# Kernel tuning notes

Measured on AMD Instinct MI355X. Metric: run time of the kernel, lower is better.

Reference implementation:

```python
import jax, jax.numpy as jnp
import numpy as np
from jax import lax

# Dimensions (see shape_source): CAML on MIMIC-style ICD coding
B, L, D, F, Y, V, K = 8, 2500, 100, 50, 8000, 50002, 9
PAD = K // 2  # floor(kernel_size/2) = 4 -> 'same' length for odd K


def setup_inputs() -> dict:
    key = jax.random.key(0)
    ks = jax.random.split(key, 8)
    x = jax.random.randint(ks[0], (B, L), 0, V)                      # token ids
    target = (jax.random.uniform(ks[1], (B, Y)) < 0.01).astype(jnp.float32)  # sparse multi-label
    embed_W = (jax.random.normal(ks[2], (V, D)) * 0.1).at[0].set(0.0)  # padding_idx=0 row zeroed
    conv_w = jax.random.normal(ks[3], (F, D, K)) * 0.05                # (out_ch, in_ch, k)
    conv_b = jax.random.normal(ks[4], (F,)) * 0.01
    U_w = jax.random.normal(ks[5], (Y, F)) * 0.05                      # attention; nn.Linear weight, bias unused
    final_w = jax.random.normal(ks[6], (Y, F)) * 0.05
    final_b = jax.random.normal(ks[7], (Y,)) * 0.01
    return dict(x=x, target=target, embed_W=embed_W, conv_w=conv_w,
                conv_b=conv_b, U_w=U_w, final_w=final_w, final_b=final_b)


def reference(x, target, embed_W, conv_w, conv_b, U_w, final_w, final_b):
    # embed (dropout is identity at eval)
    e = embed_W[x]                                   # (B, L, D)
    # conv1d over length, 'same' padding, then tanh
    h = lax.conv_general_dilated(
        jnp.transpose(e, (0, 2, 1)), conv_w,
        window_strides=(1,), padding=[(PAD, PAD)],
        dimension_numbers=("NCH", "OIH", "NCH"))
    h = jnp.tanh(h + conv_b[None, :, None])          # (B, F, L)
    h = jnp.transpose(h, (0, 2, 1))                  # (B, L, F)
    # label-wise attention pooling: alpha = softmax(U.weight @ h^T) over L
    scores = jnp.einsum('yf,blf->byl', U_w, h)       # (B, Y, L) -- large intermediate
    alpha = jax.nn.softmax(scores, axis=2)
    m = jnp.einsum('byl,blf->byf', alpha, h)         # (B, Y, F)
    yhat = jnp.sum(final_w[None, :, :] * m, axis=2) + final_b  # (B, Y)
    # F.binary_cross_entropy_with_logits, mean reduction (stable form)
    loss = jnp.mean(jnp.maximum(yhat, 0) - yhat * target + jnp.log1p(jnp.exp(-jnp.abs(yhat))))
    return yhat, loss, alpha
```

## Files before the change

kernel.cpp:

```cpp
#include <hip/hip_runtime.h>
#include <hip/hip_bf16.h>
#include <math.h>

#define BB 8
#define LL 2500
#define LPAD 2560
#define DD 100
#define FF 50
#define FP 64
#define YY 8000
#define KS 9
#define LCH 256
#define NCH 10

typedef __attribute__((ext_vector_type(8))) short short8;
typedef __attribute__((ext_vector_type(4))) float f32x4;
typedef float f32x4u __attribute__((ext_vector_type(4), aligned(4)));

__device__ inline f32x4 mfma_bf16(short8 a, short8 b, f32x4 c) {
    return __builtin_amdgcn_mfma_f32_16x16x32_bf16(a, b, c, 0, 0, 0);
}

__device__ inline unsigned short f2bf(float x) {
    unsigned int u = __builtin_bit_cast(unsigned int, x);
    unsigned int r = u + 0x7fffu + ((u >> 16) & 1u);
    return (unsigned short)(r >> 16);
}

__device__ inline unsigned long long pack4bf(const float* a) {
    return (unsigned long long)f2bf(a[0])
         | ((unsigned long long)f2bf(a[1]) << 16)
         | ((unsigned long long)f2bf(a[2]) << 32)
         | ((unsigned long long)f2bf(a[3]) << 48);
}

__device__ inline float bf2f(unsigned short s) {
    return __builtin_bit_cast(float, (unsigned int)s << 16);
}

__device__ inline float tanhfast(float x) {
    float e = __expf(2.f * x);
    return 1.f - 2.f / (e + 1.f);
}

__global__ void k_prep(const float* __restrict__ cw, unsigned short* __restrict__ wA,
                       const float* __restrict__ Uw, unsigned short* __restrict__ Ub) {
    int i = blockIdx.x * blockDim.x + threadIdx.x;
    if (i < 64 * KS * 128) {
        int f = i / (KS * 128);
        int r = i - f * (KS * 128);
        int kk = r >> 7;
        int d = r & 127;
        float v = (f < FF && d < DD) ? cw[(f * DD + d) * KS + kk] : 0.f;
        wA[i] = f2bf(v);
    }
    if (i < YY * FP) {
        int y = i >> 6, f = i & 63;
        float v = (f < FF) ? Uw[y * FF + f] : 0.f;
        Ub[i] = f2bf(v);
    }
}

__global__ __launch_bounds__(256) void k_conv(const int* __restrict__ x,
                                              const float* __restrict__ embW,
                                              const unsigned short* __restrict__ wA,
                                              const float* __restrict__ cb,
                                              unsigned short* __restrict__ hB,
                                              unsigned short* __restrict__ hT) {
    __shared__ unsigned short eL[72 * 136];
    __shared__ int sX[72];
    int b = blockIdx.x & 7;
    int t = blockIdx.x >> 3;
    int l0 = t * 64;
    int tid = threadIdx.x;

    if (tid < 72) {
        int gl = l0 - 4 + tid;
        sX[tid] = (gl >= 0 && gl < LL) ? x[b * LL + gl] : -1;
    }
    __syncthreads();
    for (int i = tid; i < 72 * 25; i += 256) {
        int row = i / 25, c = i - row * 25;
        int id = sX[row];
        float4 v = make_float4(0.f, 0.f, 0.f, 0.f);
        if (id >= 0) v = *(const float4*)(embW + (size_t)id * DD + c * 4);
        float a[4] = {v.x, v.y, v.z, v.w};
        *(unsigned long long*)&eL[row * 136 + c * 4] = pack4bf(a);
    }
    for (int i = tid; i < 72 * 9; i += 256) {
        int row = i / 9, c = i - row * 9;
        *(unsigned long long*)&eL[row * 136 + 100 + c * 4] = 0ull;
    }
    __syncthreads();

    int w = tid >> 6, lane = tid & 63, lm = lane & 15, g = lane >> 4;
    f32x4 cacc[4];
#pragma unroll
    for (int mt = 0; mt < 4; ++mt) cacc[mt] = (f32x4){0.f, 0.f, 0.f, 0.f};

    for (int kk = 0; kk < KS; ++kk) {
#pragma unroll
        for (int dc = 0; dc < 4; ++dc) {
            short8 bfrag = *(const short8*)&eL[(w * 16 + lm + kk) * 136 + dc * 32 + g * 8];
#pragma unroll
            for (int mt = 0; mt < 4; ++mt) {
                short8 afrag = *(const short8*)(wA + ((mt * 16 + lm) * KS + kk) * 128 + dc * 32 + g * 8);
                cacc[mt] = mfma_bf16(afrag, bfrag, cacc[mt]);
            }
        }
    }

    int l = l0 + w * 16 + lm;
    unsigned long long packs[4];
#pragma unroll
    for (int mt = 0; mt < 4; ++mt) {
        float vals[4];
#pragma unroll
        for (int j = 0; j < 4; ++j) {
            int f = mt * 16 + g * 4 + j;
            vals[j] = (f < FF) ? tanhfast(cacc[mt][j] + cb[f]) : 0.f;
        }
        packs[mt] = pack4bf(vals);
        *(unsigned long long*)&hB[((size_t)b * LPAD + l) * FP + mt * 16 + g * 4] = packs[mt];
    }
    __syncthreads();
    unsigned short* hTile = eL;
#pragma unroll
    for (int mt = 0; mt < 4; ++mt)
#pragma unroll
        for (int j = 0; j < 4; ++j)
            hTile[(mt * 16 + g * 4 + j) * 72 + w * 16 + lm] =
                (unsigned short)(packs[mt] >> (16 * j));
    __syncthreads();
    {
        int f = tid >> 2, q = tid & 3;
        short8 v0 = *(const short8*)&hTile[f * 72 + q * 16];
        short8 v1 = *(const short8*)&hTile[f * 72 + q * 16 + 8];
        unsigned short* dst = hT + ((size_t)b * FP + f) * LPAD + l0 + q * 16;
        *(short8*)dst = v0;
        *(short8*)(dst + 8) = v1;
    }
}

__global__ __launch_bounds__(256, 4) void k_attn7(const unsigned short* __restrict__ hB,
                                                  const unsigned short* __restrict__ hT,
                                                  const unsigned short* __restrict__ Ub,
                                                  const float* __restrict__ fw,
                                                  const float* __restrict__ fb,
                                                  const float* __restrict__ tgt,
                                                  float* __restrict__ out,
                                                  float* __restrict__ lossAcc) {
    __shared__ unsigned short sAB[2][32 * LCH];
    __shared__ float sRed[128];
    __shared__ float sInv[32];

    int b = blockIdx.x & 7;
    int y0 = (blockIdx.x >> 3) * 32;
    int tid = threadIdx.x;
    int w = tid >> 6, lane = tid & 63, lm = lane & 15, g = lane >> 4;

    const unsigned short* hBb = hB + (size_t)b * LPAD * FP;
    const unsigned short* hTb = hT + (size_t)b * FP * LPAD;

    short8 uf[2][2];
#pragma unroll
    for (int yt = 0; yt < 2; ++yt) {
        uf[yt][0] = *(const short8*)(Ub + (size_t)(y0 + yt * 16 + lm) * FP + g * 8);
        uf[yt][1] = *(const short8*)(Ub + (size_t)(y0 + yt * 16 + lm) * FP + 32 + g * 8);
    }

    float ssum[2] = {0.f, 0.f};
    for (int it = 0; it < 40; ++it) {
        int l0 = it * 64 + w * 16;
        const unsigned short* hrow = hBb + (size_t)l0 * FP;
        short8 a0 = *(const short8*)(hrow + lm * FP + g * 8);
        short8 a1 = *(const short8*)(hrow + lm * FP + 32 + g * 8);
#pragma unroll
        for (int yt = 0; yt < 2; ++yt) {
            f32x4 cc = {0.f, 0.f, 0.f, 0.f};
            cc = mfma_bf16(a0, uf[yt][0], cc);
            cc = mfma_bf16(a1, uf[yt][1], cc);
#pragma unroll
            for (int j = 0; j < 4; ++j)
                ssum[yt] += (l0 + g * 4 + j < LL) ? __expf(cc[j]) : 0.f;
        }
    }
#pragma unroll
    for (int yt = 0; yt < 2; ++yt) {
        float s = ssum[yt];
        s += __shfl_xor(s, 16);
        s += __shfl_xor(s, 32);
        if (g == 0) sRed[w * 32 + yt * 16 + lm] = s;
    }
    __syncthreads();
    if (tid < 32)
        sInv[tid] = 1.f / (sRed[tid] + sRed[32 + tid] + sRed[64 + tid] + sRed[96 + tid]);
    __syncthreads();

    f32x4 macc[2][4];
#pragma unroll
    for (int yt = 0; yt < 2; ++yt)
#pragma unroll
        for (int ft = 0; ft < 4; ++ft) macc[yt][ft] = (f32x4){0.f, 0.f, 0.f, 0.f};

    float* alphaBase = out + 64001 + ((size_t)b * YY + y0) * LL;
    int buf = 0;
    for (int c = 0; c < NCH; ++c) {
        char* sw = (char*)sAB[buf];
#pragma unroll
        for (int t = 0; t < 4; ++t) {
            int lt = w * 4 + t;
            int l0 = c * LCH + lt * 16;
            const unsigned short* hrow = hBb + (size_t)l0 * FP;
            short8 a0 = *(const short8*)(hrow + lm * FP + g * 8);
            short8 a1 = *(const short8*)(hrow + lm * FP + 32 + g * 8);
#pragma unroll
            for (int yt = 0; yt < 2; ++yt) {
                f32x4 cc = {0.f, 0.f, 0.f, 0.f};
                cc = mfma_bf16(a0, uf[yt][0], cc);
                cc = mfma_bf16(a1, uf[yt][1], cc);
                float inv = sInv[yt * 16 + lm];
                float av[4];
#pragma unroll
                for (int j = 0; j < 4; ++j)
                    av[j] = (l0 + g * 4 + j < LL) ? __expf(cc[j]) * inv : 0.f;
                int row = yt * 16 + lm;
                int off = row * 512 + ((lt * 32 + g * 8) ^ ((lm & 7) << 4));
                *(unsigned long long*)&sw[off] = pack4bf(av);
            }
        }
        __syncthreads();
#pragma unroll
        for (int rr = 0; rr < 8; ++rr) {
            int row = w * 8 + rr;
            int lc = lane * 4;
            if (c * LCH + lc < LL) {
                unsigned long long pv =
                    *(const unsigned long long*)&sw[row * 512 + ((lane * 8) ^ ((row & 7) << 4))];
                f32x4 v = {bf2f((unsigned short)pv),
                           bf2f((unsigned short)(pv >> 16)),
                           bf2f((unsigned short)(pv >> 32)),
                           bf2f((unsigned short)(pv >> 48))};
                __builtin_nontemporal_store(v,
                    (f32x4u*)(alphaBase + (size_t)row * LL + c * LCH + lc));
            }
        }
#pragma unroll
        for (int i = 0; i < 2; ++i) {
            int kc = w * 2 + i;
            short8 bf[4];
#pragma unroll
            for (int ft = 0; ft < 4; ++ft)
                bf[ft] = *(const short8*)(hTb + (size_t)(ft * 16 + lm) * LPAD + c * LCH + kc * 32 + g * 8);
#pragma unroll
            for (int yt = 0; yt < 2; ++yt) {
                int row = yt * 16 + lm;
                short8 pa = *(const short8*)&sw[row * 512 + ((kc * 64 + g * 16) ^ ((lm & 7) << 4))];
#pragma unroll
                for (int ft = 0; ft < 4; ++ft)
                    macc[yt][ft] = mfma_bf16(pa, bf[ft], macc[yt][ft]);
            }
        }
        buf ^= 1;
    }

#pragma unroll
    for (int yt = 0; yt < 2; ++yt) {
#pragma unroll
        for (int j = 0; j < 4; ++j) {
            int y = y0 + yt * 16 + g * 4 + j;
            float z = 0.f;
#pragma unroll
            for (int ft = 0; ft < 4; ++ft) {
                int f = ft * 16 + lm;
                float fwv = (f < FF) ? fw[(size_t)y * FF + f] : 0.f;
                z += macc[yt][ft][j] * fwv;
            }
            z += __shfl_xor(z, 1);
            z += __shfl_xor(z, 2);
            z += __shfl_xor(z, 4);
            z += __shfl_xor(z, 8);
            if (lm == 0) sRed[w * 32 + yt * 16 + g * 4 + j] = z;
        }
    }
    __syncthreads();
    if (w == 0) {
        float bce = 0.f;
        if (lane < 32) {
            int y = y0 + lane;
            float z = sRed[lane] + sRed[32 + lane] + sRed[64 + lane] + sRed[96 + lane] + fb[y];
            out[b * YY + y] = z;
            float tg = tgt[b * YY + y];
            bce = fmaxf(z, 0.f) - z * tg + log1pf(__expf(-fabsf(z)));
        }
        bce += __shfl_xor(bce, 1);
        bce += __shfl_xor(bce, 2);
        bce += __shfl_xor(bce, 4);
        bce += __shfl_xor(bce, 8);
        bce += __shfl_xor(bce, 16);
        bce += __shfl_xor(bce, 32);
        if (lane == 0) atomicAdd(lossAcc, bce);
    }
}

__global__ void k_loss(const float* __restrict__ acc, float* __restrict__ out) {
    out[64000] = acc[0] / (float)(BB * YY);
}

extern "C" void kernel_launch(void* const* d_in, const int* in_sizes, int n_in,
                              void* d_out, int out_size, void* d_ws, size_t ws_size,
                              hipStream_t stream) {
    const int*   x    = (const int*)d_in[0];
    const float* tgt  = (const float*)d_in[1];
    const float* embW = (const float*)d_in[2];
    const float* cw   = (const float*)d_in[3];
    const float* cb   = (const float*)d_in[4];
    const float* Uw   = (const float*)d_in[5];
    const float* fw   = (const float*)d_in[6];
    const float* fb   = (const float*)d_in[7];
    float* out = (float*)d_out;

    float*          lossAcc = (float*)d_ws;
    unsigned short* wA = (unsigned short*)((char*)d_ws + 256);
    unsigned short* Ub = (unsigned short*)((char*)d_ws + 163840);
    unsigned short* hB = (unsigned short*)((char*)d_ws + 1212416);
    unsigned short* hT = (unsigned short*)((char*)d_ws + 3833856);

    hipMemsetAsync(d_ws, 0, 4, stream);
    k_prep<<<(YY * FP + 255) / 256, 256, 0, stream>>>(cw, wA, Uw, Ub);
    k_conv<<<BB * 40, 256, 0, stream>>>(x, embW, wA, cb, hB, hT);
    k_attn7<<<250 * 8, 256, 0, stream>>>(hB, hT, Ub, fw, fb, tgt, out, lossAcc);
    k_loss<<<1, 1, 0, stream>>>(lossAcc, out);
}
```

Baseline: 307.2 us.

## Split softmax denominator into separate kernel and halve attention L-chunk size

Moves the softmax denominator pass out of the attention kernel into a new k_denom kernel that writes per-(b,y) inverse sums to workspace. The attention kernel then reads these inverses directly and uses 128-wide L chunks instead of 256, which halves LDS usage so the launch bound can rise to 6 blocks per CU. The goal is higher occupancy and less in-kernel synchronization, at the cost of an extra launch and a workspace round trip, while the score matmul and exp for the denominator are still computed once in each kernel.

```diff
diff --git a/kernel.cpp b/kernel.cpp
--- a/kernel.cpp
+++ b/kernel.cpp
@@ -10,8 +10,8 @@
 #define FP 64
 #define YY 8000
 #define KS 9
-#define LCH 256
-#define NCH 10
+#define LCH 128
+#define NCH 20
 
 typedef __attribute__((ext_vector_type(8))) short short8;
 typedef __attribute__((ext_vector_type(4))) float f32x4;
@@ -142,9 +142,41 @@
     }
 }
 
-__global__ __launch_bounds__(256, 4) void k_attn7(const unsigned short* __restrict__ hB,
+__global__ __launch_bounds__(256) void k_denom(const unsigned short* __restrict__ hB,
+                                               const unsigned short* __restrict__ Ub,
+                                               float* __restrict__ invD) {
+    int b = blockIdx.x & 7;
+    int y0 = (blockIdx.x >> 3) * 64;
+    int tid = threadIdx.x;
+    int w = tid >> 6, lane = tid & 63, lm = lane & 15, g = lane >> 4;
+    int ybase = y0 + w * 16;
+
+    const unsigned short* hBb = hB + (size_t)b * LPAD * FP;
+    short8 uf0 = *(const short8*)(Ub + (size_t)(ybase + lm) * FP + g * 8);
+    short8 uf1 = *(const short8*)(Ub + (size_t)(ybase + lm) * FP + 32 + g * 8);
+
+    float ssum = 0.f;
+    for (int it = 0; it < 160; ++it) {
+        int l0 = it * 16;
+        const unsigned short* hrow = hBb + (size_t)l0 * FP;
+        short8 a0 = *(const short8*)(hrow + lm * FP + g * 8);
+        short8 a1 = *(const short8*)(hrow + lm * FP + 32 + g * 8);
+        f32x4 cc = {0.f, 0.f, 0.f, 0.f};
+        cc = mfma_bf16(a0, uf0, cc);
+        cc = mfma_bf16(a1, uf1, cc);
+#pragma unroll
+        for (int j = 0; j < 4; ++j)
+            ssum += (l0 + g * 4 + j < LL) ? __expf(cc[j]) : 0.f;
+    }
+    ssum += __shfl_xor(ssum, 16);
+    ssum += __shfl_xor(ssum, 32);
+    if (g == 0) invD[(size_t)b * YY + ybase + lm] = 1.f / ssum;
+}
+
+__global__ __launch_bounds__(256, 6) void k_attn8(const unsigned short* __restrict__ hB,
                                                   const unsigned short* __restrict__ hT,
                                                   const unsigned short* __restrict__ Ub,
+                                                  const float* __restrict__ invD,
                                                   const float* __restrict__ fw,
                                                   const float* __restrict__ fb,
                                                   const float* __restrict__ tgt,
@@ -152,7 +184,6 @@
                                                   float* __restrict__ lossAcc) {
     __shared__ unsigned short sAB[2][32 * LCH];
     __shared__ float sRed[128];
-    __shared__ float sInv[32];
 
     int b = blockIdx.x & 7;
     int y0 = (blockIdx.x >> 3) * 32;
@@ -163,39 +194,13 @@
     const unsigned short* hTb = hT + (size_t)b * FP * LPAD;
 
     short8 uf[2][2];
+    float inv[2];
 #pragma unroll
     for (int yt = 0; yt < 2; ++yt) {
         uf[yt][0] = *(const short8*)(Ub + (size_t)(y0 + yt * 16 + lm) * FP + g * 8);
         uf[yt][1] = *(const short8*)(Ub + (size_t)(y0 + yt * 16 + lm) * FP + 32 + g * 8);
-    }
-
-    float ssum[2] = {0.f, 0.f};
-    for (int it = 0; it < 40; ++it) {
-        int l0 = it * 64 + w * 16;
-        const unsigned short* hrow = hBb + (size_t)l0 * FP;
-        short8 a0 = *(const short8*)(hrow + lm * FP + g * 8);
-        short8 a1 = *(const short8*)(hrow + lm * FP + 32 + g * 8);
-#pragma unroll
-        for (int yt = 0; yt < 2; ++yt) {
-            f32x4 cc = {0.f, 0.f, 0.f, 0.f};
-            cc = mfma_bf16(a0, uf[yt][0], cc);
-            cc = mfma_bf16(a1, uf[yt][1], cc);
-#pragma unroll
-            for (int j = 0; j < 4; ++j)
-                ssum[yt] += (l0 + g * 4 + j < LL) ? __expf(cc[j]) : 0.f;
-        }
-    }
-#pragma unroll
-    for (int yt = 0; yt < 2; ++yt) {
-        float s = ssum[yt];
-        s += __shfl_xor(s, 16);
-        s += __shfl_xor(s, 32);
-        if (g == 0) sRed[w * 32 + yt * 16 + lm] = s;
-    }
-    __syncthreads();
-    if (tid < 32)
-        sInv[tid] = 1.f / (sRed[tid] + sRed[32 + tid] + sRed[64 + tid] + sRed[96 + tid]);
-    __syncthreads();
+        inv[yt] = invD[(size_t)b * YY + y0 + yt * 16 + lm];
+    }
 
     f32x4 macc[2][4];
 #pragma unroll
@@ -208,8 +213,8 @@
     for (int c = 0; c < NCH; ++c) {
         char* sw = (char*)sAB[buf];
 #pragma unroll
-        for (int t = 0; t < 4; ++t) {
-            int lt = w * 4 + t;
+        for (int t = 0; t < 2; ++t) {
+            int lt = w * 2 + t;
             int l0 = c * LCH + lt * 16;
             const unsigned short* hrow = hBb + (size_t)l0 * FP;
             short8 a0 = *(const short8*)(hrow + lm * FP + g * 8);
@@ -219,35 +224,33 @@
                 f32x4 cc = {0.f, 0.f, 0.f, 0.f};
                 cc = mfma_bf16(a0, uf[yt][0], cc);
                 cc = mfma_bf16(a1, uf[yt][1], cc);
-                float inv = sInv[yt * 16 + lm];
                 float av[4];
 #pragma unroll
                 for (int j = 0; j < 4; ++j)
-                    av[j] = (l0 + g * 4 + j < LL) ? __expf(cc[j]) * inv : 0.f;
+                    av[j] = (l0 + g * 4 + j < LL) ? __expf(cc[j]) * inv[yt] : 0.f;
                 int row = yt * 16 + lm;
-                int off = row * 512 + ((lt * 32 + g * 8) ^ ((lm & 7) << 4));
+                int off = row * 256 + ((lt * 32 + g * 8) ^ ((lm & 7) << 4));
                 *(unsigned long long*)&sw[off] = pack4bf(av);
             }
         }
         __syncthreads();
 #pragma unroll
-        for (int rr = 0; rr < 8; ++rr) {
-            int row = w * 8 + rr;
-            int lc = lane * 4;
-            if (c * LCH + lc < LL) {
-                unsigned long long pv =
-                    *(const unsigned long long*)&sw[row * 512 + ((lane * 8) ^ ((row & 7) << 4))];
+        for (int s = 0; s < 4; ++s) {
+            int row = w * 8 + s * 2 + (lane >> 5);
+            int colf = (lane & 31) * 4;
+            if (c * LCH + colf < LL) {
+                unsigned long long pv = *(const unsigned long long*)
+                    &sw[row * 256 + (((lane & 31) * 8) ^ ((row & 7) << 4))];
                 f32x4 v = {bf2f((unsigned short)pv),
                            bf2f((unsigned short)(pv >> 16)),
                            bf2f((unsigned short)(pv >> 32)),
                            bf2f((unsigned short)(pv >> 48))};
                 __builtin_nontemporal_store(v,
-                    (f32x4u*)(alphaBase + (size_t)row * LL + c * LCH + lc));
-            }
-        }
-#pragma unroll
-        for (int i = 0; i < 2; ++i) {
-            int kc = w * 2 + i;
+                    (f32x4u*)(alphaBase + (size_t)row * LL + c * LCH + colf));
+            }
+        }
+        {
+            int kc = w;
             short8 bf[4];
 #pragma unroll
             for (int ft = 0; ft < 4; ++ft)
@@ -255,7 +258,7 @@
 #pragma unroll
             for (int yt = 0; yt < 2; ++yt) {
                 int row = yt * 16 + lm;
-                short8 pa = *(const short8*)&sw[row * 512 + ((kc * 64 + g * 16) ^ ((lm & 7) << 4))];
+                short8 pa = *(const short8*)&sw[row * 256 + ((kc * 64 + g * 16) ^ ((lm & 7) << 4))];
 #pragma unroll
                 for (int ft = 0; ft < 4; ++ft)
                     macc[yt][ft] = mfma_bf16(pa, bf[ft], macc[yt][ft]);
@@ -321,14 +324,16 @@
     float* out = (float*)d_out;
 
     float*          lossAcc = (float*)d_ws;
-    unsigned short* wA = (unsigned short*)((char*)d_ws + 256);
-    unsigned short* Ub = (unsigned short*)((char*)d_ws + 163840);
-    unsigned short* hB = (unsigned short*)((char*)d_ws + 1212416);
-    unsigned short* hT = (unsigned short*)((char*)d_ws + 3833856);
+    unsigned short* wA   = (unsigned short*)((char*)d_ws + 256);
+    unsigned short* Ub   = (unsigned short*)((char*)d_ws + 147712);
+    float*          invD = (float*)((char*)d_ws + 1171712);
+    unsigned short* hB   = (unsigned short*)((char*)d_ws + 1427712);
+    unsigned short* hT   = (unsigned short*)((char*)d_ws + 4049152);
 
     hipMemsetAsync(d_ws, 0, 4, stream);
     k_prep<<<(YY * FP + 255) / 256, 256, 0, stream>>>(cw, wA, Uw, Ub);
     k_conv<<<BB * 40, 256, 0, stream>>>(x, embW, wA, cb, hB, hT);
-    k_attn7<<<250 * 8, 256, 0, stream>>>(hB, hT, Ub, fw, fb, tgt, out, lossAcc);
+    k_denom<<<125 * 8, 256, 0, stream>>>(hB, Ub, invD);
+    k_attn8<<<250 * 8, 256, 0, stream>>>(hB, hT, Ub, invD, fw, fb, tgt, out, lossAcc);
     k_loss<<<1, 1, 0, stream>>>(lossAcc, out);
 }
```

After: 454.4 us. 47.9% more time.
